# Kernel optimization log

Measured on AMD Instinct MI355X. Metric: run time of the kernel, lower is better.

Reference implementation:

```python
import jax, jax.numpy as jnp
import numpy as np

B, S, D, H = 4, 2048, 512, 8
HD = D // H
POOL_HEADS = 8


def setup_inputs() -> dict:
    key = jax.random.key(0)
    ks = iter(jax.random.split(key, 32))
    p = {}
    p['x'] = jax.random.normal(next(ks), (B, S, D), dtype=jnp.float32)
    p['mask'] = jnp.zeros((B, S), dtype=jnp.float32)  # key_padding_mask (1.0 = padded)
    s = 1.0 / np.sqrt(D)
    for layer in ('1', '2'):
        for name in ('q', 'k', 'v', 'o'):
            p[f'{name}{layer}_w'] = jax.random.normal(next(ks), (D, D), dtype=jnp.float32) * s
            p[f'{name}{layer}_b'] = jnp.zeros((D,), dtype=jnp.float32)
    p['ln1_g'] = jnp.ones((D,), jnp.float32); p['ln1_b'] = jnp.zeros((D,), jnp.float32)
    p['ffn_w1'] = jax.random.normal(next(ks), (D, D), dtype=jnp.float32) * s
    p['ffn_b1'] = jnp.zeros((D,), jnp.float32)
    p['ffn_w2'] = jax.random.normal(next(ks), (D, D), dtype=jnp.float32) * s
    p['ffn_b2'] = jnp.zeros((D,), jnp.float32)
    p['ln2_g'] = jnp.ones((D,), jnp.float32); p['ln2_b'] = jnp.zeros((D,), jnp.float32)
    p['pool_w'] = jax.random.normal(next(ks), (D, POOL_HEADS), dtype=jnp.float32) * s
    p['pool_b'] = jnp.zeros((POOL_HEADS,), jnp.float32)
    return p


def _layernorm(x, g, b, eps=1e-5):
    mu = jnp.mean(x, axis=-1, keepdims=True)
    var = jnp.var(x, axis=-1, keepdims=True)
    return (x - mu) * jax.lax.rsqrt(var + eps) * g + b


def _mha(x, mask, qw, qb, kw, kb, vw, vb, ow, ob):
    b, s, d = x.shape
    q = (x @ qw + qb).reshape(b, s, H, HD)
    k = (x @ kw + kb).reshape(b, s, H, HD)
    v = (x @ vw + vb).reshape(b, s, H, HD)
    scores = jnp.einsum('bihd,bjhd->bhij', q, k) / jnp.sqrt(jnp.float32(HD))
    scores = scores - mask[:, None, None, :] * 1e30  # key_padding_mask
    w = jax.nn.softmax(scores, axis=-1)  # dropout is identity at eval
    out = jnp.einsum('bhij,bjhd->bihd', w, v).reshape(b, s, d)
    return out @ ow + ob


def _pool(x, mask, pw, pb):
    alpha = jax.nn.leaky_relu(x @ pw + pb)            # [B,S,POOL_HEADS]
    alpha = alpha + mask[:, :, None] * -1e16
    alpha = jax.nn.softmax(alpha, axis=1)             # softmax over sequence
    # sum over heads of alpha_h * x, then sum over sequence
    return jnp.einsum('bs,bsd->bd', alpha.sum(axis=-1), x)


def reference(x, mask,
              q1_w, q1_b, k1_w, k1_b, v1_w, v1_b, o1_w, o1_b,
              q2_w, q2_b, k2_w, k2_b, v2_w, v2_b, o2_w, o2_b,
              ln1_g, ln1_b, ffn_w1, ffn_b1, ffn_w2, ffn_b2,
              ln2_g, ln2_b, pool_w, pool_b):
    # F.normalize(x, p=2, dim=-1)
    x = x / jnp.maximum(jnp.linalg.norm(x, axis=-1, keepdims=True), 1e-12)
    h = _mha(x, mask, q1_w, q1_b, k1_w, k1_b, v1_w, v1_b, o1_w, o1_b)
    h = _layernorm(h, ln1_g, ln1_b)
    h = jax.nn.relu(h @ ffn_w1 + ffn_b1) @ ffn_w2 + ffn_b2
    h = _mha(h, mask, q2_w, q2_b, k2_w, k2_b, v2_w, v2_b, o2_w, o2_b)
    h = _layernorm(h, ln2_g, ln2_b)
    return _pool(h, mask, pool_w, pool_b)  # [B, D] patch_feature (cls=False -> logit is None)
```

## Files before the change

### kernel.cpp

```cpp
#include <hip/hip_runtime.h>
#include <hip/hip_bf16.h>
#include <stdint.h>

#define DEVI __device__ __forceinline__

typedef float f32x4 __attribute__((ext_vector_type(4)));
typedef float f32x16 __attribute__((ext_vector_type(16)));
typedef short bf16x8 __attribute__((ext_vector_type(8)));

typedef __attribute__((address_space(3))) unsigned int as3_u32;
typedef __attribute__((address_space(1))) unsigned int as1_u32;

DEVI void gload16(const void* g, void* l) {
  __builtin_amdgcn_global_load_lds((const as1_u32*)g, (as3_u32*)l, 16, 0, 0);
}

DEVI unsigned short bf16r(float f) {
  union { float f; unsigned int u; } v; v.f = f;
  unsigned int u = v.u;
  return (unsigned short)((u + 0x7FFFu + ((u >> 16) & 1u)) >> 16);
}

DEVI float bf2f(unsigned short u) {
  unsigned int x = ((unsigned int)u) << 16;
  union { unsigned int u; float f; } v; v.u = x;
  return v.f;
}

DEVI unsigned int pkbf16(float a, float b) {
  __hip_bfloat162 h = __float22bfloat162_rn(make_float2(a, b));
  return *(unsigned int*)&h;
}

struct PrepArgs {
  const float* w[10];
  const float* b1[3];
  const float* b2[3];
};

__global__ __launch_bounds__(256) void prep_l2norm_kernel(PrepArgs pa, unsigned short* wt,
                                                          float* qb1, float* qb2,
                                                          const float* __restrict__ x,
                                                          unsigned short* __restrict__ xn) {
  const int bid = blockIdx.x;
  if (bid < 640) {
    __shared__ float lt[64][65];
    const int slot = bid >> 6, r = bid & 63;
    const int n0 = (r & 7) * 64, k0 = (r >> 3) * 64;
    const float* W = pa.w[slot];
    for (int it = 0; it < 16; it++) {
      int idx = it * 256 + threadIdx.x;
      int kr = idx >> 6, nc = idx & 63;
      lt[kr][nc] = W[(long)(k0 + kr) * 512 + n0 + nc];
    }
    __syncthreads();
    unsigned short* dst = wt + (long)slot * 512 * 512;
    for (int it = 0; it < 16; it++) {
      int idx = it * 256 + threadIdx.x;
      int nr = idx >> 6, kc = idx & 63;
      dst[(long)(n0 + nr) * 512 + k0 + kc] = bf16r(lt[kc][nr]);
    }
    if (r == 0) {
      if (slot < 3) {
        for (int i = threadIdx.x; i < 512; i += 256) qb1[slot * 512 + i] = pa.b1[slot][i];
      } else if (slot >= 6 && slot < 9) {
        for (int i = threadIdx.x; i < 512; i += 256) qb2[(slot - 6) * 512 + i] = pa.b2[slot - 6][i];
      }
    }
  } else {
    const long row = bid - 640;
    const float* xr = x + row * 512;
    float v0 = xr[threadIdx.x], v1 = xr[threadIdx.x + 256];
    float ss = v0 * v0 + v1 * v1;
    #pragma unroll
    for (int off = 32; off > 0; off >>= 1) ss += __shfl_down(ss, off, 64);
    __shared__ float red[4];
    __shared__ float sc[1];
    int w = threadIdx.x >> 6, ln = threadIdx.x & 63;
    if (ln == 0) red[w] = ss;
    __syncthreads();
    if (threadIdx.x == 0) {
      float S = red[0] + red[1] + red[2] + red[3];
      sc[0] = 1.0f / fmaxf(sqrtf(S), 1e-12f);
    }
    __syncthreads();
    float s = sc[0];
    xn[row * 512 + threadIdx.x] = bf16r(v0 * s);
    xn[row * 512 + threadIdx.x + 256] = bf16r(v1 * s);
  }
}

template <int EPI>
__global__ __launch_bounds__(256) void gemm64(const unsigned short* __restrict__ A,
                                              const unsigned short* __restrict__ Bt,
                                              const float* __restrict__ bias,
                                              void* __restrict__ Cv, int K, int N,
                                              unsigned short* __restrict__ vtout) {
  __shared__ unsigned short ldsA[64 * 64];
  __shared__ unsigned short ldsB[64 * 64];
  const int tid = threadIdx.x, w = tid >> 6, ln = tid & 63;
  const int bm = blockIdx.x, bn = blockIdx.y;
  const int wm = (w >> 1) * 32, wn = (w & 1) * 32;
  const f32x4 zf = {0.f, 0.f, 0.f, 0.f};
  f32x4 acc[2][2];
  #pragma unroll
  for (int i = 0; i < 2; i++)
    #pragma unroll
    for (int j = 0; j < 2; j++) acc[i][j] = zf;
  const int r8 = ln >> 3, s8 = ln & 7;
  for (int kt = 0; kt < K; kt += 64) {
    #pragma unroll
    for (int u = 0; u < 4; u++) {
      int jj = w * 4 + u;
      if (jj < 8) {
        gload16(A + (long)(bm * 64 + jj * 8 + r8) * K + kt + s8 * 8, &ldsA[jj * 512]);
      } else {
        int jb = jj - 8;
        gload16(Bt + (long)(bn * 64 + jb * 8 + r8) * K + kt + s8 * 8, &ldsB[jb * 512]);
      }
    }
    __syncthreads();
    #pragma unroll
    for (int kk = 0; kk < 2; kk++) {
      bf16x8 af[2], bfr[2];
      #pragma unroll
      for (int mf = 0; mf < 2; mf++)
        af[mf] = *(const bf16x8*)&ldsA[(wm + mf * 16 + (ln & 15)) * 64 + kk * 32 + (ln >> 4) * 8];
      #pragma unroll
      for (int nf = 0; nf < 2; nf++)
        bfr[nf] = *(const bf16x8*)&ldsB[(wn + nf * 16 + (ln & 15)) * 64 + kk * 32 + (ln >> 4) * 8];
      #pragma unroll
      for (int mf = 0; mf < 2; mf++)
        #pragma unroll
        for (int nf = 0; nf < 2; nf++)
          acc[mf][nf] = __builtin_amdgcn_mfma_f32_16x16x32_bf16(af[mf], bfr[nf], acc[mf][nf], 0, 0, 0);
    }
    __syncthreads();
  }
  const int g = ln >> 4, c = ln & 15;
  #pragma unroll
  for (int mf = 0; mf < 2; mf++) {
    #pragma unroll
    for (int nf = 0; nf < 2; nf++) {
      int col = bn * 64 + wn + nf * 16 + c;
      float bv = bias[col];
      if (EPI == 3 && col >= 1024) {
        long row0 = bm * 64 + wm + mf * 16 + g * 4;
        int b = (int)(row0 >> 11), s = (int)(row0 & 2047);
        int vc = col - 1024, h = vc >> 6, hd = vc & 63;
        ushort4 o;
        o.x = bf16r(acc[mf][nf][0] + bv);
        o.y = bf16r(acc[mf][nf][1] + bv);
        o.z = bf16r(acc[mf][nf][2] + bv);
        o.w = bf16r(acc[mf][nf][3] + bv);
        *(ushort4*)(vtout + ((long)((b * 8 + h) * 64 + hd)) * 2048 + s) = o;
      } else {
        #pragma unroll
        for (int j = 0; j < 4; j++) {
          long row = bm * 64 + wm + mf * 16 + g * 4 + j;
          float v = acc[mf][nf][j] + bv;
          if (EPI == 2) v = v > 0.f ? v : 0.f;
          ((unsigned short*)Cv)[row * N + col] = bf16r(v);
        }
      }
    }
  }
}

__global__ __launch_bounds__(256, 4) void attn_kernel(
    const unsigned short* __restrict__ qkv,
    const unsigned short* __restrict__ vt,
    const float* __restrict__ mask,
    unsigned short* __restrict__ ao) {
  const int tid = threadIdx.x, w = tid >> 6, ln = tid & 63;
  const int lo = ln & 31, hi = ln >> 5;
  const int bid = blockIdx.x + 16 * blockIdx.y;
  const int swz = (bid & 7) * 64 + (bid >> 3);
  const int qb = swz & 15, bh = swz >> 4;
  const int b = bh >> 3, h = bh & 7;
  const int q0 = qb * 128 + w * 32;
  const unsigned short* qp = qkv + (long)(b * 2048) * 1536 + h * 64;
  const unsigned short* kp = qp + 512;
  const unsigned short* vtp = vt + (long)bh * 64 * 2048;
  const float* mp = mask + b * 2048;

  __shared__ unsigned short sbuf[2][4096];
  __shared__ float mbuf[2048];
  __shared__ int mflag;

  {
    float acc = 0.f;
    #pragma unroll
    for (int i = 0; i < 8; i++) {
      float mv = mp[i * 256 + tid];
      mbuf[i * 256 + tid] = mv;
      acc += fabsf(mv);
    }
    if (tid == 0) mflag = 0;
    __syncthreads();
    if (acc != 0.f) mflag = 1;
    __syncthreads();
  }
  const bool anymask = (mflag != 0);

  const int jj0 = w * 2;
  const char *src0, *src1;
  long step;
  if (w < 2) {
    int r0 = jj0 * 8 + (ln >> 3), r1 = r0 + 8, s = ln & 7;
    src0 = (const char*)kp + 2L * ((long)r0 * 1536 + ((s ^ (r0 & 7)) * 8));
    src1 = (const char*)kp + 2L * ((long)r1 * 1536 + ((s ^ (r1 & 7)) * 8));
    step = 32L * 1536 * 2;
  } else {
    int j0 = (w - 2) * 2;
    int r0 = j0 * 16 + (ln >> 2), r1 = r0 + 16, s = ln & 3;
    src0 = (const char*)vtp + 2L * ((long)r0 * 2048 + ((s ^ ((r0 >> 1) & 3)) * 8));
    src1 = (const char*)vtp + 2L * ((long)r1 * 2048 + ((s ^ ((r1 >> 1) & 3)) * 8));
    step = 64;
  }
  unsigned short* const d0a = &sbuf[0][jj0 * 512];
  unsigned short* const d0b = d0a + 512;
  unsigned short* const d1a = &sbuf[1][jj0 * 512];
  unsigned short* const d1b = d1a + 512;

  int koffe[4];
  #pragma unroll
  for (int t = 0; t < 4; t++)
    koffe[t] = lo * 64 + (((t * 2 + hi) ^ (lo & 7)) * 8);
  int voffe[4];
  #pragma unroll
  for (int stt = 0; stt < 2; stt++)
    #pragma unroll
    for (int tau = 0; tau < 2; tau++) {
      int vr = tau * 32 + lo;
      voffe[stt * 2 + tau] = 2048 + vr * 32 + ((((stt * 2 + hi) ^ ((vr >> 1) & 3))) * 8);
    }

  bf16x8 qf[4];
  #pragma unroll
  for (int t = 0; t < 4; t++)
    qf[t] = *(const bf16x8*)(qp + (long)(q0 + lo) * 1536 + t * 16 + hi * 8);

  f32x16 oacc[2];
  #pragma unroll
  for (int t = 0; t < 2; t++)
    #pragma unroll
    for (int r = 0; r < 16; r++) oacc[t][r] = 0.f;
  float lsum = 0.f;
  const f32x16 zf16 = oacc[0];
  const float SC = 0.18033688011112042f;

  gload16(src0, d0a);
  gload16(src1, d0b);
  src0 += step; src1 += step;

#define ATTN_BODY(CURB, DA, DB, ITOFF, STAGE_NEXT)                              \
  {                                                                             \
    if (STAGE_NEXT) {                                                           \
      gload16(src0, DA);                                                        \
      gload16(src1, DB);                                                        \
      src0 += step; src1 += step;                                               \
      asm volatile("s_waitcnt vmcnt(2)" ::: "memory");                          \
    } else {                                                                    \
      asm volatile("s_waitcnt vmcnt(0)" ::: "memory");                          \
    }                                                                           \
    __builtin_amdgcn_s_barrier();                                               \
    __builtin_amdgcn_sched_barrier(0);                                          \
    f32x16 sacc = zf16;                                                         \
    _Pragma("unroll")                                                           \
    for (int t = 0; t < 4; t++) {                                               \
      bf16x8 kf = *(const bf16x8*)&sbuf[CURB][koffe[t]];                        \
      sacc = __builtin_amdgcn_mfma_f32_32x32x16_bf16(kf, qf[t], sacc, 0, 0, 0); \
    }                                                                           \
    float e[16];                                                                \
    _Pragma("unroll")                                                           \
    for (int r = 0; r < 16; r++) e[r] = sacc[r] * SC;                           \
    if (anymask) {                                                              \
      float mval = mbuf[(ITOFF) + lo];                                          \
      _Pragma("unroll")                                                         \
      for (int r = 0; r < 16; r++)                                              \
        e[r] -= 1.4426950408889634e30f *                                        \
                __shfl(mval, (r & 3) + 8 * (r >> 2) + 4 * hi, 64);              \
    }                                                                           \
    _Pragma("unroll")                                                           \
    for (int r = 0; r < 16; r++) e[r] = __builtin_amdgcn_exp2f(e[r]);           \
    _Pragma("unroll")                                                           \
    for (int r = 0; r < 16; r++) lsum += e[r];                                  \
    unsigned int cv[8];                                                         \
    _Pragma("unroll")                                                           \
    for (int i = 0; i < 8; i++) cv[i] = pkbf16(e[2 * i], e[2 * i + 1]);         \
    _Pragma("unroll")                                                           \
    for (int stt = 0; stt < 2; stt++) {                                         \
      unsigned int pf[4];                                                       \
      {                                                                         \
        auto r0_ = __builtin_amdgcn_permlane32_swap(cv[stt * 4 + 0],            \
                                                    cv[stt * 4 + 2], false, false); \
        auto r1_ = __builtin_amdgcn_permlane32_swap(cv[stt * 4 + 1],            \
                                                    cv[stt * 4 + 3], false, false); \
        pf[0] = r0_[0]; pf[1] = r1_[0]; pf[2] = r0_[1]; pf[3] = r1_[1];         \
      }                                                                         \
      bf16x8 pfr = *(const bf16x8*)pf;                                          \
      _Pragma("unroll")                                                         \
      for (int tau = 0; tau < 2; tau++) {                                       \
        bf16x8 vf = *(const bf16x8*)&sbuf[CURB][voffe[stt * 2 + tau]];          \
        oacc[tau] = __builtin_amdgcn_mfma_f32_32x32x16_bf16(vf, pfr, oacc[tau], 0, 0, 0); \
      }                                                                         \
    }                                                                           \
    __builtin_amdgcn_sched_barrier(0);                                          \
    __builtin_amdgcn_s_barrier();                                               \
  }

  for (int it2 = 0; it2 < 32; it2++) {
    ATTN_BODY(0, d1a, d1b, it2 * 64, 1)
    ATTN_BODY(1, d0a, d0b, it2 * 64 + 32, (it2 < 31))
  }
#undef ATTN_BODY

  lsum += __shfl_xor(lsum, 32, 64);
  const float inv = 1.f / lsum;
  unsigned short* ob = ao + ((long)(b * 2048) + q0 + lo) * 512 + h * 64;
  #pragma unroll
  for (int tau = 0; tau < 2; tau++) {
    #pragma unroll
    for (int j = 0; j < 4; j++) {
      ushort4 o;
      o.x = bf16r(oacc[tau][4 * j + 0] * inv);
      o.y = bf16r(oacc[tau][4 * j + 1] * inv);
      o.z = bf16r(oacc[tau][4 * j + 2] * inv);
      o.w = bf16r(oacc[tau][4 * j + 3] * inv);
      *(ushort4*)(ob + tau * 32 + j * 8 + hi * 4) = o;
    }
  }
}

__global__ __launch_bounds__(256) void ln_kernel(const unsigned short* __restrict__ in,
                                                 const float* __restrict__ gam,
                                                 const float* __restrict__ bet,
                                                 unsigned short* __restrict__ out) {
  const long row = blockIdx.x;
  const unsigned short* x = in + row * 512;
  float v0 = bf2f(x[threadIdx.x]), v1 = bf2f(x[threadIdx.x + 256]);
  float s = v0 + v1, ss = v0 * v0 + v1 * v1;
  #pragma unroll
  for (int off = 32; off > 0; off >>= 1) {
    s += __shfl_down(s, off, 64);
    ss += __shfl_down(ss, off, 64);
  }
  __shared__ float red[8];
  __shared__ float mv[2];
  int w = threadIdx.x >> 6, ln = threadIdx.x & 63;
  if (ln == 0) { red[w] = s; red[w + 4] = ss; }
  __syncthreads();
  if (threadIdx.x == 0) {
    float S = red[0] + red[1] + red[2] + red[3];
    float SS = red[4] + red[5] + red[6] + red[7];
    float mu = S * (1.f / 512.f);
    float var = SS * (1.f / 512.f) - mu * mu;
    mv[0] = mu;
    mv[1] = rsqrtf(var + 1e-5f);
  }
  __syncthreads();
  float mu = mv[0], rs = mv[1];
  float o0 = (v0 - mu) * rs * gam[threadIdx.x] + bet[threadIdx.x];
  float o1 = (v1 - mu) * rs * gam[threadIdx.x + 256] + bet[threadIdx.x + 256];
  out[row * 512 + threadIdx.x] = bf16r(o0);
  out[row * 512 + threadIdx.x + 256] = bf16r(o1);
}

__global__ __launch_bounds__(256) void ln2_alpha_kernel(const unsigned short* __restrict__ in,
                                                        const float* __restrict__ gam,
                                                        const float* __restrict__ bet,
                                                        const float* __restrict__ pw,
                                                        const float* __restrict__ pbias,
                                                        const float* __restrict__ mask,
                                                        unsigned short* __restrict__ out,
                                                        float* __restrict__ alpha) {
  const long row = blockIdx.x;
  const unsigned short* x = in + row * 512;
  float v0 = bf2f(x[threadIdx.x]), v1 = bf2f(x[threadIdx.x + 256]);
  float s = v0 + v1, ss = v0 * v0 + v1 * v1;
  #pragma unroll
  for (int off = 32; off > 0; off >>= 1) {
    s += __shfl_down(s, off, 64);
    ss += __shfl_down(ss, off, 64);
  }
  __shared__ float red[8];
  __shared__ float mv[2];
  __shared__ float pr[4][8];
  int w = threadIdx.x >> 6, ln = threadIdx.x & 63;
  if (ln == 0) { red[w] = s; red[w + 4] = ss; }
  __syncthreads();
  if (threadIdx.x == 0) {
    float S = red[0] + red[1] + red[2] + red[3];
    float SS = red[4] + red[5] + red[6] + red[7];
    float mu = S * (1.f / 512.f);
    float var = SS * (1.f / 512.f) - mu * mu;
    mv[0] = mu;
    mv[1] = rsqrtf(var + 1e-5f);
  }
  __syncthreads();
  float mu = mv[0], rs = mv[1];
  float o0 = (v0 - mu) * rs * gam[threadIdx.x] + bet[threadIdx.x];
  float o1 = (v1 - mu) * rs * gam[threadIdx.x + 256] + bet[threadIdx.x + 256];
  out[row * 512 + threadIdx.x] = bf16r(o0);
  out[row * 512 + threadIdx.x + 256] = bf16r(o1);
  float p[8];
  const float* w0 = pw + threadIdx.x * 8;
  const float* w1 = pw + (threadIdx.x + 256) * 8;
  #pragma unroll
  for (int k = 0; k < 8; k++) p[k] = o0 * w0[k] + o1 * w1[k];
  #pragma unroll
  for (int off = 32; off > 0; off >>= 1)
    #pragma unroll
    for (int k = 0; k < 8; k++) p[k] += __shfl_down(p[k], off, 64);
  if (ln == 0)
    #pragma unroll
    for (int k = 0; k < 8; k++) pr[w][k] = p[k];
  __syncthreads();
  if (threadIdx.x < 8) {
    float a = pr[0][threadIdx.x] + pr[1][threadIdx.x] + pr[2][threadIdx.x] + pr[3][threadIdx.x]
              + pbias[threadIdx.x];
    a = a < 0.f ? 0.01f * a : a;
    alpha[row * 8 + threadIdx.x] = a + mask[row] * (-1e16f);
  }
}

__global__ __launch_bounds__(256) void pool_kernel(const unsigned short* __restrict__ h,
                                                   const float* __restrict__ alpha,
                                                   float* __restrict__ partial) {
  int b = blockIdx.x >> 3, sc = blockIdx.x & 7;
  int w = threadIdx.x >> 6, ln = threadIdx.x & 63;
  __shared__ float red[4][8];
  __shared__ float Ms[8], Ss[8];
  __shared__ float wb[256];
  const float* ab = alpha + (long)b * 2048 * 8;
  float m[8];
  #pragma unroll
  for (int k = 0; k < 8; k++) m[k] = -1e38f;
  for (int s = threadIdx.x; s < 2048; s += 256) {
    const float* a = ab + (long)s * 8;
    #pragma unroll
    for (int k = 0; k < 8; k++) m[k] = fmaxf(m[k], a[k]);
  }
  #pragma unroll
  for (int off = 32; off > 0; off >>= 1)
    #pragma unroll
    for (int k = 0; k < 8; k++) m[k] = fmaxf(m[k], __shfl_down(m[k], off, 64));
  if (ln == 0)
    #pragma unroll
    for (int k = 0; k < 8; k++) red[w][k] = m[k];
  __syncthreads();
  if (threadIdx.x < 8)
    Ms[threadIdx.x] = fmaxf(fmaxf(red[0][threadIdx.x], red[1][threadIdx.x]),
                            fmaxf(red[2][threadIdx.x], red[3][threadIdx.x]));
  __syncthreads();
  float sm[8];
  #pragma unroll
  for (int k = 0; k < 8; k++) sm[k] = 0.f;
  for (int s = threadIdx.x; s < 2048; s += 256) {
    const float* a = ab + (long)s * 8;
    #pragma unroll
    for (int k = 0; k < 8; k++) sm[k] += __expf(a[k] - Ms[k]);
  }
  #pragma unroll
  for (int off = 32; off > 0; off >>= 1)
    #pragma unroll
    for (int k = 0; k < 8; k++) sm[k] += __shfl_down(sm[k], off, 64);
  __syncthreads();
  if (ln == 0)
    #pragma unroll
    for (int k = 0; k < 8; k++) red[w][k] = sm[k];
  __syncthreads();
  if (threadIdx.x < 8)
    Ss[threadIdx.x] = red[0][threadIdx.x] + red[1][threadIdx.x] +
                      red[2][threadIdx.x] + red[3][threadIdx.x];
  __syncthreads();
  int s0 = sc * 256;
  {
    const float* a = ab + (long)(s0 + threadIdx.x) * 8;
    float wsum = 0.f;
    #pragma unroll
    for (int ph = 0; ph < 8; ph++) wsum += __expf(a[ph] - Ms[ph]) / Ss[ph];
    wb[threadIdx.x] = wsum;
  }
  __syncthreads();
  float a0 = 0.f, a1 = 0.f;
  const unsigned short* hb = h + ((long)b * 2048 + s0) * 512;
  for (int i = 0; i < 256; i++) {
    float wv = wb[i];
    a0 += wv * bf2f(hb[(long)i * 512 + threadIdx.x]);
    a1 += wv * bf2f(hb[(long)i * 512 + threadIdx.x + 256]);
  }
  partial[(long)blockIdx.x * 512 + threadIdx.x] = a0;
  partial[(long)blockIdx.x * 512 + threadIdx.x + 256] = a1;
}

__global__ __launch_bounds__(256) void pool_final(const float* __restrict__ partial,
                                                  float* __restrict__ out) {
  int b = blockIdx.x;
  float a0 = 0.f, a1 = 0.f;
  #pragma unroll
  for (int sc = 0; sc < 8; sc++) {
    a0 += partial[(long)(b * 8 + sc) * 512 + threadIdx.x];
    a1 += partial[(long)(b * 8 + sc) * 512 + threadIdx.x + 256];
  }
  out[b * 512 + threadIdx.x] = a0;
  out[b * 512 + threadIdx.x + 256] = a1;
}

extern "C" void kernel_launch(void* const* d_in, const int* in_sizes, int n_in,
                              void* d_out, int out_size, void* d_ws, size_t ws_size,
                              hipStream_t stream) {
  (void)in_sizes; (void)n_in; (void)out_size;
  if (ws_size < 92274688UL) return;

  const float* x    = (const float*)d_in[0];
  const float* mask = (const float*)d_in[1];
  const float* q1w = (const float*)d_in[2];  const float* q1b = (const float*)d_in[3];
  const float* k1w = (const float*)d_in[4];  const float* k1b = (const float*)d_in[5];
  const float* v1w = (const float*)d_in[6];  const float* v1b = (const float*)d_in[7];
  const float* o1w = (const float*)d_in[8];  const float* o1b = (const float*)d_in[9];
  const float* q2w = (const float*)d_in[10]; const float* q2b = (const float*)d_in[11];
  const float* k2w = (const float*)d_in[12]; const float* k2b = (const float*)d_in[13];
  const float* v2w = (const float*)d_in[14]; const float* v2b = (const float*)d_in[15];
  const float* o2w = (const float*)d_in[16]; const float* o2b = (const float*)d_in[17];
  const float* ln1g = (const float*)d_in[18]; const float* ln1b = (const float*)d_in[19];
  const float* fw1 = (const float*)d_in[20]; const float* fb1 = (const float*)d_in[21];
  const float* fw2 = (const float*)d_in[22]; const float* fb2 = (const float*)d_in[23];
  const float* ln2g = (const float*)d_in[24]; const float* ln2b = (const float*)d_in[25];
  const float* poolw = (const float*)d_in[26]; const float* poolb = (const float*)d_in[27];

  char* ws = (char*)d_ws;
  unsigned short* Wt  = (unsigned short*)(ws + 0);
  float* qb1          = (float*)(ws + 5242880);
  float* qb2          = (float*)(ws + 5249024);
  float* alpha        = (float*)(ws + 5255424);
  float* partial      = (float*)(ws + 5517568);
  unsigned short* qkv = (unsigned short*)(ws + 8388608);
  unsigned short* vt  = (unsigned short*)(ws + 33554432);
  unsigned short* ao  = (unsigned short*)(ws + 41943040);
  unsigned short* tb  = (unsigned short*)(ws + 50331648);
  unsigned short* xn  = (unsigned short*)(ws + 67108864);
  unsigned short* h1  = (unsigned short*)(ws + 75497472);
  unsigned short* f   = (unsigned short*)(ws + 83886080);
  unsigned short* h2  = xn;

  PrepArgs pa;
  pa.w[0] = q1w; pa.w[1] = k1w; pa.w[2] = v1w; pa.w[3] = o1w; pa.w[4] = fw1;
  pa.w[5] = fw2; pa.w[6] = q2w; pa.w[7] = k2w; pa.w[8] = v2w; pa.w[9] = o2w;
  pa.b1[0] = q1b; pa.b1[1] = k1b; pa.b1[2] = v1b;
  pa.b2[0] = q2b; pa.b2[1] = k2b; pa.b2[2] = v2b;

  prep_l2norm_kernel<<<8832, 256, 0, stream>>>(pa, Wt, qb1, qb2, x, xn);

  gemm64<3><<<dim3(128, 24), 256, 0, stream>>>(xn, Wt, qb1, qkv, 512, 1536, vt);
  attn_kernel<<<dim3(16, 32), 256, 0, stream>>>(qkv, vt, mask, ao);
  gemm64<1><<<dim3(128, 8), 256, 0, stream>>>(ao, Wt + 3L * 512 * 512, o1b, tb, 512, 512, nullptr);
  ln_kernel<<<8192, 256, 0, stream>>>(tb, ln1g, ln1b, h1);
  gemm64<2><<<dim3(128, 8), 256, 0, stream>>>(h1, Wt + 4L * 512 * 512, fb1, f, 512, 512, nullptr);
  gemm64<1><<<dim3(128, 8), 256, 0, stream>>>(f, Wt + 5L * 512 * 512, fb2, h2, 512, 512, nullptr);

  gemm64<3><<<dim3(128, 24), 256, 0, stream>>>(h2, Wt + 6L * 512 * 512, qb2, qkv, 512, 1536, vt);
  attn_kernel<<<dim3(16, 32), 256, 0, stream>>>(qkv, vt, mask, ao);
  gemm64<1><<<dim3(128, 8), 256, 0, stream>>>(ao, Wt + 9L * 512 * 512, o2b, tb, 512, 512, nullptr);
  ln2_alpha_kernel<<<8192, 256, 0, stream>>>(tb, ln2g, ln2b, poolw, poolb, mask, tb, alpha);

  pool_kernel<<<32, 256, 0, stream>>>(tb, alpha, partial);
  pool_final<<<4, 256, 0, stream>>>(partial, (float*)d_out);
}
```

Measured before the change: 275.8 us.

## Process two 32-row query tiles per wave in attention to reuse K/V fragments

Each attention wave now handles 64 query rows as two 32-row sub-tiles that share the same K and V fragments read from LDS. Each block therefore covers 256 queries and the grid is halved. The aim is to halve the K/V staging traffic and LDS reads per query and to give more independent MFMA chains for interleaving. In exchange, register pressure roughly doubles for accumulators and Q fragments, so launch bounds drop to 2 blocks per CU, and fewer blocks are launched overall.

Result: slower. 309.6 us (+12.3%).

```diff
diff --git a/kernel.cpp b/kernel.cpp
--- a/kernel.cpp
+++ b/kernel.cpp
@@ -167,18 +167,18 @@
   }
 }
 
-__global__ __launch_bounds__(256, 4) void attn_kernel(
+__global__ __launch_bounds__(256, 2) void attn_kernel(
     const unsigned short* __restrict__ qkv,
     const unsigned short* __restrict__ vt,
     const float* __restrict__ mask,
     unsigned short* __restrict__ ao) {
   const int tid = threadIdx.x, w = tid >> 6, ln = tid & 63;
   const int lo = ln & 31, hi = ln >> 5;
-  const int bid = blockIdx.x + 16 * blockIdx.y;
-  const int swz = (bid & 7) * 64 + (bid >> 3);
-  const int qb = swz & 15, bh = swz >> 4;
+  const int bid = blockIdx.x + 8 * blockIdx.y;
+  const int swz = (bid & 7) * 32 + (bid >> 3);
+  const int qb = swz & 7, bh = swz >> 3;
   const int b = bh >> 3, h = bh & 7;
-  const int q0 = qb * 128 + w * 32;
+  const int q0 = qb * 256 + w * 64;
   const unsigned short* qp = qkv + (long)(b * 2048) * 1536 + h * 64;
   const unsigned short* kp = qp + 512;
   const unsigned short* vtp = vt + (long)bh * 64 * 2048;
@@ -236,18 +236,20 @@
       voffe[stt * 2 + tau] = 2048 + vr * 32 + ((((stt * 2 + hi) ^ ((vr >> 1) & 3))) * 8);
     }
 
-  bf16x8 qf[4];
-  #pragma unroll
-  for (int t = 0; t < 4; t++)
-    qf[t] = *(const bf16x8*)(qp + (long)(q0 + lo) * 1536 + t * 16 + hi * 8);
-
-  f32x16 oacc[2];
+  bf16x8 qfA[4], qfB[4];
+  #pragma unroll
+  for (int t = 0; t < 4; t++) {
+    qfA[t] = *(const bf16x8*)(qp + (long)(q0 + lo) * 1536 + t * 16 + hi * 8);
+    qfB[t] = *(const bf16x8*)(qp + (long)(q0 + 32 + lo) * 1536 + t * 16 + hi * 8);
+  }
+
+  f32x16 oaccA[2], oaccB[2];
   #pragma unroll
   for (int t = 0; t < 2; t++)
     #pragma unroll
-    for (int r = 0; r < 16; r++) oacc[t][r] = 0.f;
-  float lsum = 0.f;
-  const f32x16 zf16 = oacc[0];
+    for (int r = 0; r < 16; r++) { oaccA[t][r] = 0.f; oaccB[t][r] = 0.f; }
+  float lsumA = 0.f, lsumB = 0.f;
+  const f32x16 zf16 = oaccA[0];
   const float SC = 0.18033688011112042f;
 
   gload16(src0, d0a);
@@ -266,44 +268,66 @@
     }                                                                           \
     __builtin_amdgcn_s_barrier();                                               \
     __builtin_amdgcn_sched_barrier(0);                                          \
-    f32x16 sacc = zf16;                                                         \
-    _Pragma("unroll")                                                           \
-    for (int t = 0; t < 4; t++) {                                               \
-      bf16x8 kf = *(const bf16x8*)&sbuf[CURB][koffe[t]];                        \
-      sacc = __builtin_amdgcn_mfma_f32_32x32x16_bf16(kf, qf[t], sacc, 0, 0, 0); \
-    }                                                                           \
-    float e[16];                                                                \
-    _Pragma("unroll")                                                           \
-    for (int r = 0; r < 16; r++) e[r] = sacc[r] * SC;                           \
+    bf16x8 kf[4];                                                               \
+    _Pragma("unroll")                                                           \
+    for (int t = 0; t < 4; t++)                                                 \
+      kf[t] = *(const bf16x8*)&sbuf[CURB][koffe[t]];                            \
+    f32x16 saccA = zf16, saccB = zf16;                                          \
+    _Pragma("unroll")                                                           \
+    for (int t = 0; t < 4; t++)                                                 \
+      saccA = __builtin_amdgcn_mfma_f32_32x32x16_bf16(kf[t], qfA[t], saccA, 0, 0, 0); \
+    _Pragma("unroll")                                                           \
+    for (int t = 0; t < 4; t++)                                                 \
+      saccB = __builtin_amdgcn_mfma_f32_32x32x16_bf16(kf[t], qfB[t], saccB, 0, 0, 0); \
+    float madj[16];                                                             \
     if (anymask) {                                                              \
       float mval = mbuf[(ITOFF) + lo];                                          \
       _Pragma("unroll")                                                         \
       for (int r = 0; r < 16; r++)                                              \
-        e[r] -= 1.4426950408889634e30f *                                        \
-                __shfl(mval, (r & 3) + 8 * (r >> 2) + 4 * hi, 64);              \
+        madj[r] = 1.4426950408889634e30f *                                      \
+                  __shfl(mval, (r & 3) + 8 * (r >> 2) + 4 * hi, 64);            \
+    } else {                                                                    \
+      _Pragma("unroll")                                                         \
+      for (int r = 0; r < 16; r++) madj[r] = 0.f;                               \
     }                                                                           \
-    _Pragma("unroll")                                                           \
-    for (int r = 0; r < 16; r++) e[r] = __builtin_amdgcn_exp2f(e[r]);           \
-    _Pragma("unroll")                                                           \
-    for (int r = 0; r < 16; r++) lsum += e[r];                                  \
-    unsigned int cv[8];                                                         \
-    _Pragma("unroll")                                                           \
-    for (int i = 0; i < 8; i++) cv[i] = pkbf16(e[2 * i], e[2 * i + 1]);         \
+    float e[16];                                                                \
+    unsigned int cvA[8], cvB[8];                                                \
+    _Pragma("unroll")                                                           \
+    for (int r = 0; r < 16; r++)                                                \
+      e[r] = __builtin_amdgcn_exp2f(saccA[r] * SC - madj[r]);                   \
+    _Pragma("unroll")                                                           \
+    for (int r = 0; r < 16; r++) lsumA += e[r];                                 \
+    _Pragma("unroll")                                                           \
+    for (int i = 0; i < 8; i++) cvA[i] = pkbf16(e[2 * i], e[2 * i + 1]);        \
+    _Pragma("unroll")                                                           \
+    for (int r = 0; r < 16; r++)                                                \
+      e[r] = __builtin_amdgcn_exp2f(saccB[r] * SC - madj[r]);                   \
+    _Pragma("unroll")                                                           \
+    for (int r = 0; r < 16; r++) lsumB += e[r];                                 \
+    _Pragma("unroll")                                                           \
+    for (int i = 0; i < 8; i++) cvB[i] = pkbf16(e[2 * i], e[2 * i + 1]);        \
     _Pragma("unroll")                                                           \
     for (int stt = 0; stt < 2; stt++) {                                         \
-      unsigned int pf[4];                                                       \
+      unsigned int pfA[4], pfB[4];                                              \
       {                                                                         \
-        auto r0_ = __builtin_amdgcn_permlane32_swap(cv[stt * 4 + 0],            \
-                                                    cv[stt * 4 + 2], false, false); \
-        auto r1_ = __builtin_amdgcn_permlane32_swap(cv[stt * 4 + 1],            \
-                                                    cv[stt * 4 + 3], false, false); \
-        pf[0] = r0_[0]; pf[1] = r1_[0]; pf[2] = r0_[1]; pf[3] = r1_[1];         \
+        auto rA0 = __builtin_amdgcn_permlane32_swap(cvA[stt * 4 + 0],           \
+                                                    cvA[stt * 4 + 2], false, false); \
+        auto rA1 = __builtin_amdgcn_permlane32_swap(cvA[stt * 4 + 1],           \
+                                                    cvA[stt * 4 + 3], false, false); \
+        pfA[0] = rA0[0]; pfA[1] = rA1[0]; pfA[2] = rA0[1]; pfA[3] = rA1[1];     \
+        auto rB0 = __builtin_amdgcn_permlane32_swap(cvB[stt * 4 + 0],           \
+                                                    cvB[stt * 4 + 2], false, false); \
+        auto rB1 = __builtin_amdgcn_permlane32_swap(cvB[stt * 4 + 1],           \
+                                                    cvB[stt * 4 + 3], false, false); \
+        pfB[0] = rB0[0]; pfB[1] = rB1[0]; pfB[2] = rB0[1]; pfB[3] = rB1[1];     \
       }                                                                         \
-      bf16x8 pfr = *(const bf16x8*)pf;                                          \
+      bf16x8 pfrA = *(const bf16x8*)pfA;                                        \
+      bf16x8 pfrB = *(const bf16x8*)pfB;                                        \
       _Pragma("unroll")                                                         \
       for (int tau = 0; tau < 2; tau++) {                                       \
         bf16x8 vf = *(const bf16x8*)&sbuf[CURB][voffe[stt * 2 + tau]];          \
-        oacc[tau] = __builtin_amdgcn_mfma_f32_32x32x16_bf16(vf, pfr, oacc[tau], 0, 0, 0); \
+        oaccA[tau] = __builtin_amdgcn_mfma_f32_32x32x16_bf16(vf, pfrA, oaccA[tau], 0, 0, 0); \
+        oaccB[tau] = __builtin_amdgcn_mfma_f32_32x32x16_bf16(vf, pfrB, oaccB[tau], 0, 0, 0); \
       }                                                                         \
     }                                                                           \
     __builtin_amdgcn_sched_barrier(0);                                          \
@@ -316,19 +340,27 @@
   }
 #undef ATTN_BODY
 
-  lsum += __shfl_xor(lsum, 32, 64);
-  const float inv = 1.f / lsum;
-  unsigned short* ob = ao + ((long)(b * 2048) + q0 + lo) * 512 + h * 64;
+  lsumA += __shfl_xor(lsumA, 32, 64);
+  lsumB += __shfl_xor(lsumB, 32, 64);
+  const float invA = 1.f / lsumA;
+  const float invB = 1.f / lsumB;
+  unsigned short* obA = ao + ((long)(b * 2048) + q0 + lo) * 512 + h * 64;
+  unsigned short* obB = obA + 32L * 512;
   #pragma unroll
   for (int tau = 0; tau < 2; tau++) {
     #pragma unroll
     for (int j = 0; j < 4; j++) {
-      ushort4 o;
-      o.x = bf16r(oacc[tau][4 * j + 0] * inv);
-      o.y = bf16r(oacc[tau][4 * j + 1] * inv);
-      o.z = bf16r(oacc[tau][4 * j + 2] * inv);
-      o.w = bf16r(oacc[tau][4 * j + 3] * inv);
-      *(ushort4*)(ob + tau * 32 + j * 8 + hi * 4) = o;
+      ushort4 oA, oB;
+      oA.x = bf16r(oaccA[tau][4 * j + 0] * invA);
+      oA.y = bf16r(oaccA[tau][4 * j + 1] * invA);
+      oA.z = bf16r(oaccA[tau][4 * j + 2] * invA);
+      oA.w = bf16r(oaccA[tau][4 * j + 3] * invA);
+      *(ushort4*)(obA + tau * 32 + j * 8 + hi * 4) = oA;
+      oB.x = bf16r(oaccB[tau][4 * j + 0] * invB);
+      oB.y = bf16r(oaccB[tau][4 * j + 1] * invB);
+      oB.z = bf16r(oaccB[tau][4 * j + 2] * invB);
+      oB.w = bf16r(oaccB[tau][4 * j + 3] * invB);
+      *(ushort4*)(obB + tau * 32 + j * 8 + hi * 4) = oB;
     }
   }
 }
@@ -554,14 +586,14 @@
   prep_l2norm_kernel<<<8832, 256, 0, stream>>>(pa, Wt, qb1, qb2, x, xn);
 
   gemm64<3><<<dim3(128, 24), 256, 0, stream>>>(xn, Wt, qb1, qkv, 512, 1536, vt);
-  attn_kernel<<<dim3(16, 32), 256, 0, stream>>>(qkv, vt, mask, ao);
+  attn_kernel<<<dim3(8, 32), 256, 0, stream>>>(qkv, vt, mask, ao);
   gemm64<1><<<dim3(128, 8), 256, 0, stream>>>(ao, Wt + 3L * 512 * 512, o1b, tb, 512, 512, nullptr);
   ln_kernel<<<8192, 256, 0, stream>>>(tb, ln1g, ln1b, h1);
   gemm64<2><<<dim3(128, 8), 256, 0, stream>>>(h1, Wt + 4L * 512 * 512, fb1, f, 512, 512, nullptr);
   gemm64<1><<<dim3(128, 8), 256, 0, stream>>>(f, Wt + 5L * 512 * 512, fb2, h2, 512, 512, nullptr);
 
   gemm64<3><<<dim3(128, 24), 256, 0, stream>>>(h2, Wt + 6L * 512 * 512, qb2, qkv, 512, 1536, vt);
-  attn_kernel<<<dim3(16, 32), 256, 0, stream>>>(qkv, vt, mask, ao);
+  attn_kernel<<<dim3(8, 32), 256, 0, stream>>>(qkv, vt, mask, ao);
   gemm64<1><<<dim3(128, 8), 256, 0, stream>>>(ao, Wt + 9L * 512 * 512, o2b, tb, 512, 512, nullptr);
   ln2_alpha_kernel<<<8192, 256, 0, stream>>>(tb, ln2g, ln2b, poolw, poolb, mask, tb, alpha);
 
```
